# Kernel tuning notes

Hardware: AMD Instinct MI355X
Metric: run time of the kernel (lower is better)

The kernel has to match this reference:

```python
import jax, jax.numpy as jnp
import numpy as np

WS = 7   # window_size
SS = 3   # shift_size
NH = 6   # num_heads
EPS = 1e-5


def _partition(x, ws):
    # [b,h,w,c] -> [b*(h//ws)*(w//ws), ws*ws, c]
    b, h, w, c = x.shape
    x = x.reshape(b, h // ws, ws, w // ws, ws, c)
    return x.transpose(0, 1, 3, 2, 4, 5).reshape(-1, ws * ws, c)


def _reverse(windows, ws, h, w, b):
    c = windows.shape[-1]
    x = windows.reshape(b, h // ws, w // ws, ws, ws, c)
    return x.transpose(0, 1, 3, 2, 4, 5).reshape(b, h, w, c)


def _make_mask(h, w, ws, ss):
    # static (numpy) shifted-window attention mask, [nw, ws*ws, ws*ws]
    img = np.zeros((h, w), dtype=np.float32)
    slices = (slice(0, -ws), slice(-ws, -ss), slice(-ss, None))
    cnt = 0
    for hs in slices:
        for wsl in slices:
            img[hs, wsl] = cnt
            cnt += 1
    mw = img.reshape(h // ws, ws, w // ws, ws).transpose(0, 2, 1, 3).reshape(-1, ws * ws)
    am = mw[:, None, :] - mw[:, :, None]
    mask = np.where(am != 0, -100.0, 0.0).astype(np.float32)
    return jnp.asarray(mask)


def _layernorm(x, g, b):
    mu = jnp.mean(x, axis=-1, keepdims=True)
    var = jnp.var(x, axis=-1, keepdims=True)
    return (x - mu) * jax.lax.rsqrt(var + EPS) * g + b


def setup_inputs() -> dict:
    key = jax.random.key(0)
    ks = jax.random.split(key, 8)
    dim = 192
    s = lambda fan: 1.0 / np.sqrt(fan)
    return {
        "x": jax.random.normal(ks[0], (64, 56, 56, dim), dtype=jnp.float32),
        "n1_g": jnp.ones((dim,), jnp.float32),
        "n1_b": jnp.zeros((dim,), jnp.float32),
        "qkv_w": jax.random.normal(ks[1], (dim, 3 * dim), jnp.float32) * s(dim),
        "qkv_b": jnp.zeros((3 * dim,), jnp.float32),
        "proj_w": jax.random.normal(ks[2], (dim, dim), jnp.float32) * s(dim),
        "proj_b": jnp.zeros((dim,), jnp.float32),
        "n2_g": jnp.ones((dim,), jnp.float32),
        "n2_b": jnp.zeros((dim,), jnp.float32),
        "w1": jax.random.normal(ks[3], (dim, 4 * dim), jnp.float32) * s(dim),
        "b1": jnp.zeros((4 * dim,), jnp.float32),
        "w2": jax.random.normal(ks[4], (4 * dim, dim), jnp.float32) * s(4 * dim),
        "b2": jnp.zeros((dim,), jnp.float32),
    }


def reference(x, n1_g, n1_b, qkv_w, qkv_b, proj_w, proj_b, n2_g, n2_b, w1, b1, w2, b2):
    b, h, w, c = x.shape
    hd = c // NH
    scale = hd ** -0.5

    sc = x
    xn = _layernorm(x, n1_g, n1_b)
    sx = jnp.roll(xn, shift=(-SS, -SS), axis=(1, 2))

    xw = _partition(sx, WS)                      # [B_, n, c], n = WS*WS
    B_, n, _ = xw.shape

    qkv = xw @ qkv_w + qkv_b                      # [B_, n, 3c]
    qkv = qkv.reshape(B_, n, 3, NH, hd).transpose(2, 0, 3, 1, 4)
    q, k, v = qkv[0], qkv[1], qkv[2]              # [B_, NH, n, hd]

    attn = jnp.einsum("whnd,whmd->whnm", q, k) * scale   # [B_, NH, n, n]
    mask = _make_mask(h, w, WS, SS)               # [nw, n, n]
    nw = mask.shape[0]
    attn = attn.reshape(b // nw * 1 if False else b, nw, NH, n, n) if False else attn.reshape(B_ // nw, nw, NH, n, n)
    attn = attn + mask[None, :, None, :, :]
    attn = attn.reshape(-1, NH, n, n)
    attn = jax.nn.softmax(attn, axis=-1)

    out = jnp.einsum("whnm,whmd->whnd", attn, v)  # [B_, NH, n, hd]
    out = out.transpose(0, 2, 1, 3).reshape(B_, n, c)
    out = out @ proj_w + proj_b

    sx = _reverse(out, WS, h, w, b)
    xs = jnp.roll(sx, shift=(SS, SS), axis=(1, 2))

    x2 = sc + xs
    x2n = _layernorm(x2, n2_g, n2_b)
    mlp = jax.nn.gelu(x2n @ w1 + b1, approximate=False) @ w2 + b2
    return x2 + mlp
```

## Files before the change

kernel.cpp:

```cpp
#include <hip/hip_runtime.h>

typedef __attribute__((ext_vector_type(4))) float f32x4;
typedef __attribute__((ext_vector_type(8))) short bf16x8;
typedef __attribute__((ext_vector_type(2))) unsigned int u32x2;

#define NHEAD 6

__device__ __forceinline__ unsigned short f2bf(float f){
  union{float f;unsigned int u;}c; c.f=f;
  unsigned int x=c.u;
  return (unsigned short)((x + 0x7FFFu + ((x>>16)&1u)) >> 16);
}
__device__ __forceinline__ unsigned int cvtpk(float a, float b){
  unsigned int r;
  asm("v_cvt_pk_bf16_f32 %0, %1, %2" : "=v"(r) : "v"(a), "v"(b));
  return r;
}

__global__ void wt_kernel(const float* __restrict__ w, unsigned short* __restrict__ wt,
                          int K, int N){
  int idx = blockIdx.x*256 + threadIdx.x;
  if (idx >= K*N) return;
  int k = idx / N, n = idx - k*N;
  wt[(size_t)n*K + k] = f2bf(w[idx]);
}

template<int SHIFT>
__global__ __launch_bounds__(256) void ln_kernel(const float* __restrict__ x,
    const float* __restrict__ gw, const float* __restrict__ bw,
    unsigned short* __restrict__ out){
  int tok  = blockIdx.x*4 + (threadIdx.x>>6);
  int lane = threadIdx.x & 63;
  const float* row = x + (size_t)tok*192;
  float4 v = make_float4(0.f,0.f,0.f,0.f);
  if (lane < 48) v = *(const float4*)(row + lane*4);
  float s  = v.x+v.y+v.z+v.w;
  float s2 = v.x*v.x+v.y*v.y+v.z*v.z+v.w*v.w;
  #pragma unroll
  for (int off=32; off; off>>=1){ s += __shfl_xor(s,off); s2 += __shfl_xor(s2,off); }
  float mu = s*(1.f/192.f);
  float rs = rsqrtf(s2*(1.f/192.f) - mu*mu + 1e-5f);
  size_t otok;
  if (SHIFT){
    int b = tok/3136; int hw = tok - b*3136; int h = hw/56; int w = hw - h*56;
    int hs = h-3; if (hs<0) hs += 56;
    int wsh = w-3; if (wsh<0) wsh += 56;
    int wr = hs/7, r = hs - wr*7, wc = wsh/7, c = wsh - wc*7;
    otok = ((size_t)b*64 + wr*8 + wc)*49 + r*7 + c;
  } else {
    otok = (size_t)tok;
  }
  if (lane < 48){
    int cb = lane*4;
    float4 g4 = *(const float4*)(gw + cb);
    float4 b4 = *(const float4*)(bw + cb);
    u32x2 o;
    o.x = cvtpk((v.x-mu)*rs*g4.x + b4.x, (v.y-mu)*rs*g4.y + b4.y);
    o.y = cvtpk((v.z-mu)*rs*g4.z + b4.z, (v.w-mu)*rs*g4.w + b4.w);
    *(u32x2*)(out + otok*192 + cb) = o;
  }
}

enum { EPI_QKV=0, EPI_PROJ=1, EPI_GELU=2, EPI_FINAL=3 };

__device__ __forceinline__ float gelu_fast(float v){
  float t = v*(1.59576912f + 0.07135481f*v*v);
  float e = __expf(-t);
  return v/(1.f + e);
}

__device__ __forceinline__ size_t proj_rowbase(int grow){
  int winr = grow/49; int nn = grow - winr*49;
  int b  = winr>>6; int wi = winr&63; int wr_ = wi>>3; int wc_ = wi&7;
  int r7 = nn/7;  int c7 = nn - r7*7;
  int h = wr_*7 + r7 + 3; if (h>=56) h-=56;
  int w = wc_*7 + c7 + 3; if (w>=56) w-=56;
  return (((size_t)b*3136) + h*56 + w)*192;
}

template<int EPI>
__global__ __launch_bounds__(512) void gemm_k(
    const unsigned short* __restrict__ A,
    const unsigned short* __restrict__ BT,
    const float* __restrict__ bias,
    const float* __restrict__ res,
    void* __restrict__ Cout,
    int M, int N, int Nb, int K)
{
  __shared__ unsigned short lA[256*64];
  __shared__ unsigned short lB[64*64];
  const int tid  = threadIdx.x;
  const int wave = tid>>6, lane = tid&63;
  const int wm = wave>>1, wn = wave&1;
  const int lr = lane&15, lh = lane>>4;

  int bid = blockIdx.x;
  int yb = bid/(8*Nb); int rr = bid - yb*8*Nb; int xq = rr>>3; int y8 = rr&7;
  const int m0 = (yb*8 + y8)*256, n0 = xq*64;

  f32x4 zero = {0.f,0.f,0.f,0.f};
  f32x4 acc[4][2];
  #pragma unroll
  for (int i=0;i<4;i++){ acc[i][0]=zero; acc[i][1]=zero; }

  const int row8 = tid>>3;
  const int csw  = ((tid&7) ^ (row8&7))*8;
  const unsigned short* Ag = A  + (size_t)(m0 + row8)*K + csw;
  const unsigned short* Bg = BT + (size_t)(n0 + row8)*K + csw;

  for (int kt=0; kt<K; kt+=64){
    __syncthreads();
    #pragma unroll
    for (int i=0;i<4;i++){
      __builtin_amdgcn_global_load_lds(
        (const __attribute__((address_space(1))) void*)(Ag + (size_t)i*64*K + kt),
        (__attribute__((address_space(3))) void*)(lA + i*4096 + wave*512),
        16, 0, 0);
    }
    __builtin_amdgcn_global_load_lds(
      (const __attribute__((address_space(1))) void*)(Bg + kt),
      (__attribute__((address_space(3))) void*)(lB + wave*512),
      16, 0, 0);
    __syncthreads();

    bf16x8 af[4][2], bfv[2][2];
    #pragma unroll
    for (int mi=0;mi<4;mi++)
      #pragma unroll
      for (int ks=0;ks<2;ks++){
        int arow = wm*64+mi*16+lr;
        af[mi][ks] = *(const bf16x8*)&lA[arow*64 + (((ks*4+lh) ^ (lr&7))*8)];
      }
    #pragma unroll
    for (int ni=0;ni<2;ni++)
      #pragma unroll
      for (int ks=0;ks<2;ks++){
        int brow = wn*32+ni*16+lr;
        bfv[ni][ks] = *(const bf16x8*)&lB[brow*64 + (((ks*4+lh) ^ (lr&7))*8)];
      }
    #pragma unroll
    for (int mi=0;mi<4;mi++)
      #pragma unroll
      for (int ni=0;ni<2;ni++)
        #pragma unroll
        for (int ks=0;ks<2;ks++)
          acc[mi][ni] = __builtin_amdgcn_mfma_f32_16x16x32_bf16(
              bfv[ni][ks], af[mi][ks], acc[mi][ni], 0,0,0);
  }

  if (EPI == EPI_QKV || EPI == EPI_GELU){
    __syncthreads();
    #pragma unroll
    for (int mi=0;mi<4;mi++){
      int row = wm*64 + mi*16 + lr;
      #pragma unroll
      for (int ni=0;ni<2;ni++){
        int colb = n0 + wn*32 + ni*16 + lh*4;
        float4 bv4 = *(const float4*)(bias + colb);
        float v0 = acc[mi][ni][0] + bv4.x;
        float v1 = acc[mi][ni][1] + bv4.y;
        float v2 = acc[mi][ni][2] + bv4.z;
        float v3 = acc[mi][ni][3] + bv4.w;
        u32x2 st;
        if (EPI == EPI_GELU){
          st.x = cvtpk(gelu_fast(v0), gelu_fast(v1));
          st.y = cvtpk(gelu_fast(v2), gelu_fast(v3));
        } else {
          st.x = cvtpk(v0,v1); st.y = cvtpk(v2,v3);
        }
        int c16 = wn*4 + ni*2 + (lh>>1);
        int byte = row*128 + ((c16 ^ (row&7))*16) + (lh&1)*8;
        *(u32x2*)((char*)lA + byte) = st;
      }
    }
    __syncthreads();
    #pragma unroll
    for (int rnd=0; rnd<4; ++rnd){
      int row = rnd*64 + (tid>>3);
      int chunk = tid&7;
      uint4 vv = *(const uint4*)((const char*)lA + row*128 + ((chunk ^ (row&7))*16));
      int grow = m0 + row;
      if (EPI == EPI_GELU){
        *(uint4*)((unsigned short*)Cout + (size_t)grow*N + n0 + chunk*8) = vv;
      } else {
        int winr = grow/49; int nn = grow - winr*49;
        int gcol = n0 + chunk*8;
        int which = gcol/192; int rem = gcol - which*192;
        int head = rem>>5, d = rem&31;
        *(uint4*)((unsigned short*)Cout + (size_t)winr*28224 + (size_t)which*9408
                  + head*1568 + nn*32 + d) = vv;
      }
    }
  } else {
    float* Tf = (float*)lA;
    #pragma unroll
    for (int h=0; h<2; ++h){
      __syncthreads();
      if ((wave>>2) == h){
        #pragma unroll
        for (int mi=0;mi<4;mi++){
          int lrow = (wm&1)*64 + mi*16 + lr;
          #pragma unroll
          for (int ni=0;ni<2;ni++){
            int colb = n0 + wn*32 + ni*16 + lh*4;
            float4 bv4 = *(const float4*)(bias + colb);
            float4 val = make_float4(acc[mi][ni][0]+bv4.x, acc[mi][ni][1]+bv4.y,
                                     acc[mi][ni][2]+bv4.z, acc[mi][ni][3]+bv4.w);
            int c4 = wn*8 + ni*4 + lh;
            *(float4*)&Tf[lrow*64 + ((c4 ^ (lrow&15))*4)] = val;
          }
        }
      }
      __syncthreads();
      #pragma unroll
      for (int rnd=0; rnd<4; ++rnd){
        int lrow = rnd*32 + (tid>>4);
        int chunk = tid&15;
        float4 v = *(const float4*)&Tf[lrow*64 + ((chunk ^ (lrow&15))*4)];
        int grow = m0 + h*128 + lrow;
        size_t base;
        if (EPI == EPI_FINAL) base = (size_t)grow*N + n0 + chunk*4;
        else                  base = proj_rowbase(grow) + n0 + chunk*4;
        float4 rv = *(const float4*)(res + base);
        *(float4*)((float*)Cout + base) =
            make_float4(rv.x+v.x, rv.y+v.y, rv.z+v.z, rv.w+v.w);
      }
    }
  }
}

__global__ __launch_bounds__(256) void attn_kernel(const unsigned short* __restrict__ qkv,
                                                   unsigned short* __restrict__ aout){
  __shared__ __align__(16) unsigned short ldsQK[4][4096];
  __shared__ __align__(16) unsigned short ldsV[4][2048];
  const int wave = threadIdx.x>>6, lane = threadIdx.x&63;
  const int lr = lane&15, lh = lane>>4;
  const int unit = blockIdx.x*4 + wave;
  const int win  = unit/NHEAD, head = unit - win*NHEAD;

  unsigned short* Q  = ldsQK[wave];
  unsigned short* Kl = ldsQK[wave] + 2048;
  unsigned short* P  = ldsQK[wave];
  unsigned short* Vt = ldsV[wave];

  const size_t wbase = (size_t)win*28224 + (size_t)head*1568;
  const unsigned short* gQ = qkv + wbase;
  const unsigned short* gK = qkv + wbase + 9408;
  const unsigned short* gV = qkv + wbase + 18816;

  {
    uint4 z = make_uint4(0,0,0,0);
    #pragma unroll
    for (int i=0;i<4;i++) *(uint4*)&Vt[(i*64+lane)*8] = z;
  }

  #pragma unroll
  for (int i=0;i<4;i++){
    int idx = i*64 + lane;
    if (idx < 196){
      int row = idx>>2, blk = idx&3;
      int sb = (blk ^ (row&3) ^ ((row>>2)&3));
      uint4 dq = *(const uint4*)(gQ + idx*8);
      *(uint4*)&Q[row*32 + sb*8] = dq;
      uint4 dk = *(const uint4*)(gK + idx*8);
      *(uint4*)&Kl[row*32 + sb*8] = dk;
    }
  }
  #pragma unroll
  for (int i=0;i<4;i++){
    int idx = i*64 + lane;
    if (idx < 196){
      int row = idx>>2, d0 = (idx&3)*8;
      uint4 dv = *(const uint4*)(gV + idx*8);
      unsigned int wds[4] = {dv.x, dv.y, dv.z, dv.w};
      int rb = row>>3, re = row&7;
      #pragma unroll
      for (int j=0;j<8;j++){
        unsigned short t = (unsigned short)(wds[j>>1] >> ((j&1)*16));
        Vt[(d0+j)*64 + ((rb ^ j)*8) + re] = t;
      }
    }
  }

  bf16x8 kf[4], qf[4];
  #pragma unroll
  for (int t=0;t<4;t++){
    int row = t*16 + lr;
    int off = row*32 + ((lh ^ (row&3) ^ ((row>>2)&3))*8);
    kf[t] = *(const bf16x8*)&Kl[off];
    qf[t] = *(const bf16x8*)&Q[off];
  }

  f32x4 zero = {0.f,0.f,0.f,0.f};
  f32x4 S[4][4];
  #pragma unroll
  for (int mi=0;mi<4;mi++)
    #pragma unroll
    for (int ni=0;ni<4;ni++)
      S[mi][ni] = __builtin_amdgcn_mfma_f32_16x16x32_bf16(kf[mi], qf[ni], zero, 0,0,0);

  const int wi = win & 63, wr = wi>>3, wc = wi&7;
  const bool hasmask = (wr==7) || (wc==7);
  const float scale = 0.17677669529663687f;

  #pragma unroll
  for (int ni=0;ni<4;ni++){
    int q = ni*16 + lr;
    int idq = 0;
    if (hasmask){
      int qr = q/7, qc = q - qr*7;
      int ih = (wr==7) ? ((qr>=4)?2:1) : 0;
      int iw = (wc==7) ? ((qc>=4)?2:1) : 0;
      idq = ih*3 + iw;
    }
    #pragma unroll
    for (int mi=0;mi<4;mi++){
      #pragma unroll
      for (int r=0;r<4;r++){
        int key = mi*16 + lh*4 + r;
        float s;
        if (key >= 49) s = -1e30f;
        else {
          float add = 0.f;
          if (hasmask){
            int kr = key/7, kc = key - kr*7;
            int ih = (wr==7) ? ((kr>=4)?2:1) : 0;
            int iw = (wc==7) ? ((kc>=4)?2:1) : 0;
            add = ((ih*3+iw) == idq) ? 0.f : -100.f;
          }
          s = S[mi][ni][r]*scale + add;
        }
        S[mi][ni][r] = s;
      }
    }
    float m = -1e30f;
    #pragma unroll
    for (int mi=0;mi<4;mi++)
      #pragma unroll
      for (int r=0;r<4;r++) m = fmaxf(m, S[mi][ni][r]);
    m = fmaxf(m, __shfl_xor(m, 16));
    m = fmaxf(m, __shfl_xor(m, 32));
    float sum = 0.f;
    #pragma unroll
    for (int mi=0;mi<4;mi++)
      #pragma unroll
      for (int r=0;r<4;r++){
        float p = __expf(S[mi][ni][r] - m);
        S[mi][ni][r] = p; sum += p;
      }
    sum += __shfl_xor(sum, 16);
    sum += __shfl_xor(sum, 32);
    float inv = 1.f/sum;
    #pragma unroll
    for (int mi=0;mi<4;mi++){
      int keyb = mi*16 + lh*4;
      int blk = keyb>>3, e0 = keyb&7;
      int addr = q*64 + ((blk ^ (q&7))*8) + e0;
      *(unsigned int*)&P[addr]   = cvtpk(S[mi][ni][0]*inv, S[mi][ni][1]*inv);
      *(unsigned int*)&P[addr+2] = cvtpk(S[mi][ni][2]*inv, S[mi][ni][3]*inv);
    }
  }

  bf16x8 vf[2][2];
  #pragma unroll
  for (int mt=0;mt<2;mt++)
    #pragma unroll
    for (int ks=0;ks<2;ks++){
      int row = mt*16 + lr;
      vf[mt][ks] = *(const bf16x8*)&Vt[row*64 + (((ks*4+lh) ^ (row&7))*8)];
    }
  f32x4 O[2][4];
  #pragma unroll
  for (int ni=0;ni<4;ni++){
    int q = ni*16 + lr;
    bf16x8 pf0 = *(const bf16x8*)&P[q*64 + (((0*4+lh) ^ (q&7))*8)];
    bf16x8 pf1 = *(const bf16x8*)&P[q*64 + (((1*4+lh) ^ (q&7))*8)];
    #pragma unroll
    for (int mt=0;mt<2;mt++){
      f32x4 t = __builtin_amdgcn_mfma_f32_16x16x32_bf16(vf[mt][0], pf0, zero, 0,0,0);
      O[mt][ni] = __builtin_amdgcn_mfma_f32_16x16x32_bf16(vf[mt][1], pf1, t, 0,0,0);
    }
  }

  #pragma unroll
  for (int ni=0;ni<4;ni++){
    int q = ni*16 + lr;
    if (q < 49){
      size_t ob = ((size_t)win*49 + q)*192 + head*32 + lh*4;
      #pragma unroll
      for (int mt=0;mt<2;mt++){
        u32x2 st;
        st.x = cvtpk(O[mt][ni][0], O[mt][ni][1]);
        st.y = cvtpk(O[mt][ni][2], O[mt][ni][3]);
        *(u32x2*)(aout + ob + mt*16) = st;
      }
    }
  }
}

extern "C" void kernel_launch(void* const* d_in, const int* in_sizes, int n_in,
                              void* d_out, int out_size, void* d_ws, size_t ws_size,
                              hipStream_t stream){
  (void)in_sizes; (void)n_in; (void)out_size; (void)ws_size;
  const float* x      = (const float*)d_in[0];
  const float* n1_g   = (const float*)d_in[1];
  const float* n1_b   = (const float*)d_in[2];
  const float* qkv_w  = (const float*)d_in[3];
  const float* qkv_b  = (const float*)d_in[4];
  const float* proj_w = (const float*)d_in[5];
  const float* proj_b = (const float*)d_in[6];
  const float* n2_g   = (const float*)d_in[7];
  const float* n2_b   = (const float*)d_in[8];
  const float* w1     = (const float*)d_in[9];
  const float* b1     = (const float*)d_in[10];
  const float* w2     = (const float*)d_in[11];
  const float* b2     = (const float*)d_in[12];

  char* ws = (char*)d_ws;
  unsigned short* qkvT = (unsigned short*)(ws + 0);
  unsigned short* projT= (unsigned short*)(ws + 221184);
  unsigned short* w1T  = (unsigned short*)(ws + 294912);
  unsigned short* w2T  = (unsigned short*)(ws + 589824);
  unsigned short* bufA = (unsigned short*)(ws + 884736);
  unsigned short* bufB = (unsigned short*)(ws + 77955072);
  float*          x2   = (float*)        (ws + 386236416);
  float* out = (float*)d_out;
  const int M = 200704;

  wt_kernel<<<432,256,0,stream>>>(qkv_w, qkvT, 192, 576);
  wt_kernel<<<144,256,0,stream>>>(proj_w, projT, 192, 192);
  wt_kernel<<<576,256,0,stream>>>(w1,    w1T,  192, 768);
  wt_kernel<<<576,256,0,stream>>>(w2,    w2T,  768, 192);

  ln_kernel<1><<<50176,256,0,stream>>>(x, n1_g, n1_b, bufA);
  gemm_k<EPI_QKV  ><<< 9*784, 512,0,stream>>>(bufA, qkvT, qkv_b, nullptr, bufB, M, 576, 9, 192);
  attn_kernel<<<6144,256,0,stream>>>(bufB, bufA);
  gemm_k<EPI_PROJ ><<< 3*784, 512,0,stream>>>(bufA, projT, proj_b, x, x2, M, 192, 3, 192);
  ln_kernel<0><<<50176,256,0,stream>>>(x2, n2_g, n2_b, bufA);
  gemm_k<EPI_GELU ><<<12*784, 512,0,stream>>>(bufA, w1T, b1, nullptr, bufB, M, 768, 12, 192);
  gemm_k<EPI_FINAL><<< 3*784, 512,0,stream>>>(bufB, w2T, b2, x2, out, M, 192, 3, 768);
}
```

Measured before the change: 714.0 us.

## Fuse QKV projection GEMM into windowed attention kernel per window

Replaces the separate QKV GEMM and attention kernels with one kernel that processes one window per block. Six waves compute the 49x576 QKV projection with MFMA, read the weights straight from global memory, and write Q, K and transposed V into LDS, where each wave then runs attention for one head. This removes the round trip of the large QKV intermediate through global memory and one kernel launch. In exchange, weight tiles are re-read from global (L2) memory by every block, the M dimension is padded from 49 to 64 rows, and per-block LDS use is larger, which can lower occupancy.

```diff
diff --git a/kernel.cpp b/kernel.cpp
--- a/kernel.cpp
+++ b/kernel.cpp
@@ -61,7 +61,7 @@
   }
 }
 
-enum { EPI_QKV=0, EPI_PROJ=1, EPI_GELU=2, EPI_FINAL=3 };
+enum { EPI_PROJ=1, EPI_GELU=2, EPI_FINAL=3 };
 
 __device__ __forceinline__ float gelu_fast(float v){
   float t = v*(1.59576912f + 0.07135481f*v*v);
@@ -148,7 +148,7 @@
               bfv[ni][ks], af[mi][ks], acc[mi][ni], 0,0,0);
   }
 
-  if (EPI == EPI_QKV || EPI == EPI_GELU){
+  if (EPI == EPI_GELU){
     __syncthreads();
     #pragma unroll
     for (int mi=0;mi<4;mi++){
@@ -162,12 +162,8 @@
         float v2 = acc[mi][ni][2] + bv4.z;
         float v3 = acc[mi][ni][3] + bv4.w;
         u32x2 st;
-        if (EPI == EPI_GELU){
-          st.x = cvtpk(gelu_fast(v0), gelu_fast(v1));
-          st.y = cvtpk(gelu_fast(v2), gelu_fast(v3));
-        } else {
-          st.x = cvtpk(v0,v1); st.y = cvtpk(v2,v3);
-        }
+        st.x = cvtpk(gelu_fast(v0), gelu_fast(v1));
+        st.y = cvtpk(gelu_fast(v2), gelu_fast(v3));
         int c16 = wn*4 + ni*2 + (lh>>1);
         int byte = row*128 + ((c16 ^ (row&7))*16) + (lh&1)*8;
         *(u32x2*)((char*)lA + byte) = st;
@@ -180,16 +176,7 @@
       int chunk = tid&7;
       uint4 vv = *(const uint4*)((const char*)lA + row*128 + ((chunk ^ (row&7))*16));
       int grow = m0 + row;
-      if (EPI == EPI_GELU){
-        *(uint4*)((unsigned short*)Cout + (size_t)grow*N + n0 + chunk*8) = vv;
-      } else {
-        int winr = grow/49; int nn = grow - winr*49;
-        int gcol = n0 + chunk*8;
-        int which = gcol/192; int rem = gcol - which*192;
-        int head = rem>>5, d = rem&31;
-        *(uint4*)((unsigned short*)Cout + (size_t)winr*28224 + (size_t)which*9408
-                  + head*1568 + nn*32 + d) = vv;
-      }
+      *(uint4*)((unsigned short*)Cout + (size_t)grow*N + n0 + chunk*8) = vv;
     }
   } else {
     float* Tf = (float*)lA;
@@ -229,58 +216,96 @@
   }
 }
 
-__global__ __launch_bounds__(256) void attn_kernel(const unsigned short* __restrict__ qkv,
-                                                   unsigned short* __restrict__ aout){
-  __shared__ __align__(16) unsigned short ldsQK[4][4096];
-  __shared__ __align__(16) unsigned short ldsV[4][2048];
-  const int wave = threadIdx.x>>6, lane = threadIdx.x&63;
+__global__ __launch_bounds__(384) void qkv_attn(
+    const unsigned short* __restrict__ xw,
+    const unsigned short* __restrict__ qkvT,
+    const float* __restrict__ bias,
+    unsigned short* __restrict__ aout)
+{
+  __shared__ __align__(16) unsigned short smem[36864];
+  const int tid  = threadIdx.x;
+  const int wave = tid>>6, lane = tid&63;
   const int lr = lane&15, lh = lane>>4;
-  const int unit = blockIdx.x*4 + wave;
-  const int win  = unit/NHEAD, head = unit - win*NHEAD;
-
-  unsigned short* Q  = ldsQK[wave];
-  unsigned short* Kl = ldsQK[wave] + 2048;
-  unsigned short* P  = ldsQK[wave];
-  unsigned short* Vt = ldsV[wave];
-
-  const size_t wbase = (size_t)win*28224 + (size_t)head*1568;
-  const unsigned short* gQ = qkv + wbase;
-  const unsigned short* gK = qkv + wbase + 9408;
-  const unsigned short* gV = qkv + wbase + 18816;
-
-  {
-    uint4 z = make_uint4(0,0,0,0);
-    #pragma unroll
-    for (int i=0;i<4;i++) *(uint4*)&Vt[(i*64+lane)*8] = z;
-  }
-
-  #pragma unroll
-  for (int i=0;i<4;i++){
-    int idx = i*64 + lane;
-    if (idx < 196){
-      int row = idx>>2, blk = idx&3;
-      int sb = (blk ^ (row&3) ^ ((row>>2)&3));
-      uint4 dq = *(const uint4*)(gQ + idx*8);
-      *(uint4*)&Q[row*32 + sb*8] = dq;
-      uint4 dk = *(const uint4*)(gK + idx*8);
-      *(uint4*)&Kl[row*32 + sb*8] = dk;
-    }
-  }
-  #pragma unroll
-  for (int i=0;i<4;i++){
-    int idx = i*64 + lane;
-    if (idx < 196){
-      int row = idx>>2, d0 = (idx&3)*8;
-      uint4 dv = *(const uint4*)(gV + idx*8);
-      unsigned int wds[4] = {dv.x, dv.y, dv.z, dv.w};
-      int rb = row>>3, re = row&7;
-      #pragma unroll
-      for (int j=0;j<8;j++){
-        unsigned short t = (unsigned short)(wds[j>>1] >> ((j&1)*16));
-        Vt[(d0+j)*64 + ((rb ^ j)*8) + re] = t;
-      }
-    }
-  }
+  const int win = blockIdx.x;
+  unsigned short* xwl = smem;
+  const size_t xbase = (size_t)win*49*192;
+
+  #pragma unroll
+  for (int p=0; p<4; ++p){
+    int c = p*384 + tid;
+    int row = c/24, col = c - row*24;
+    unsigned short* dst = &xwl[row*192 + ((col ^ (row&7))*8)];
+    if (row < 49){
+      *(uint4*)dst = *(const uint4*)(xw + xbase + (size_t)row*192 + col*8);
+    } else {
+      *(uint4*)dst = make_uint4(0,0,0,0);
+    }
+  }
+  __syncthreads();
+
+  f32x4 zero = {0.f,0.f,0.f,0.f};
+  f32x4 acc[4][6];
+  #pragma unroll
+  for (int i=0;i<4;i++)
+    #pragma unroll
+    for (int j=0;j<6;j++) acc[i][j]=zero;
+  const int ncol0 = wave*96;
+
+  #pragma unroll
+  for (int kk=0; kk<6; ++kk){
+    bf16x8 af[4];
+    #pragma unroll
+    for (int mi=0;mi<4;mi++)
+      af[mi] = *(const bf16x8*)&xwl[(mi*16+lr)*192 + (((kk*4+lh) ^ (lr&7))*8)];
+    bf16x8 bfv[6];
+    #pragma unroll
+    for (int j=0;j<6;j++)
+      bfv[j] = *(const bf16x8*)(qkvT + (size_t)(ncol0 + j*16 + lr)*192 + kk*32 + lh*8);
+    #pragma unroll
+    for (int mi=0;mi<4;mi++)
+      #pragma unroll
+      for (int j=0;j<6;j++)
+        acc[mi][j] = __builtin_amdgcn_mfma_f32_16x16x32_bf16(
+            bfv[j], af[mi], acc[mi][j], 0,0,0);
+  }
+  __syncthreads();
+
+  const int which = wave>>1;
+  #pragma unroll
+  for (int j=0;j<6;j++){
+    int unit = j>>1, ni_u = j&1;
+    int head = (wave&1)*3 + unit;
+    int d0 = ni_u*16 + lh*4;
+    float4 bb = *(const float4*)(bias + which*192 + head*32 + d0);
+    #pragma unroll
+    for (int mi=0;mi<4;mi++){
+      int row = mi*16 + lr;
+      float v0 = acc[mi][j][0]+bb.x, v1 = acc[mi][j][1]+bb.y;
+      float v2 = acc[mi][j][2]+bb.z, v3 = acc[mi][j][3]+bb.w;
+      if (which < 2){
+        unsigned short* base = smem + head*4096 + which*2048;
+        int blk = d0>>3;
+        int sb = blk ^ (row&3) ^ ((row>>2)&3);
+        int addr = row*32 + sb*8 + (d0&7);
+        u32x2 st; st.x = cvtpk(v0,v1); st.y = cvtpk(v2,v3);
+        *(u32x2*)(base + addr) = st;
+      } else {
+        unsigned short* vt = smem + 24576 + head*2048;
+        int rb = row>>3, re = row&7;
+        vt[(d0+0)*64 + ((rb ^ ((d0+0)&7))*8) + re] = f2bf(v0);
+        vt[(d0+1)*64 + ((rb ^ ((d0+1)&7))*8) + re] = f2bf(v1);
+        vt[(d0+2)*64 + ((rb ^ ((d0+2)&7))*8) + re] = f2bf(v2);
+        vt[(d0+3)*64 + ((rb ^ ((d0+3)&7))*8) + re] = f2bf(v3);
+      }
+    }
+  }
+  __syncthreads();
+
+  const int head = wave;
+  unsigned short* Q  = smem + head*4096;
+  unsigned short* Kl = Q + 2048;
+  unsigned short* P  = Q;
+  unsigned short* Vt = smem + 24576 + head*2048;
 
   bf16x8 kf[4], qf[4];
   #pragma unroll
@@ -291,7 +316,6 @@
     qf[t] = *(const bf16x8*)&Q[off];
   }
 
-  f32x4 zero = {0.f,0.f,0.f,0.f};
   f32x4 S[4][4];
   #pragma unroll
   for (int mi=0;mi<4;mi++)
@@ -433,9 +457,8 @@
   wt_kernel<<<576,256,0,stream>>>(w2,    w2T,  768, 192);
 
   ln_kernel<1><<<50176,256,0,stream>>>(x, n1_g, n1_b, bufA);
-  gemm_k<EPI_QKV  ><<< 9*784, 512,0,stream>>>(bufA, qkvT, qkv_b, nullptr, bufB, M, 576, 9, 192);
-  attn_kernel<<<6144,256,0,stream>>>(bufB, bufA);
-  gemm_k<EPI_PROJ ><<< 3*784, 512,0,stream>>>(bufA, projT, proj_b, x, x2, M, 192, 3, 192);
+  qkv_attn<<<4096,384,0,stream>>>(bufA, qkvT, qkv_b, bufB);
+  gemm_k<EPI_PROJ ><<< 3*784, 512,0,stream>>>(bufB, projT, proj_b, x, x2, M, 192, 3, 192);
   ln_kernel<0><<<50176,256,0,stream>>>(x2, n2_g, n2_b, bufA);
   gemm_k<EPI_GELU ><<<12*784, 512,0,stream>>>(bufA, w1T, b1, nullptr, bufB, M, 768, 12, 192);
   gemm_k<EPI_FINAL><<< 3*784, 512,0,stream>>>(bufB, w2T, b2, x2, out, M, 192, 3, 768);
```

New measurement: 811.7 us. 1.14x slower.

## Chunk QKV/attention and MLP stages into quarters to keep intermediates cache-resident

Applied to the files above, without the earlier changes.

Splits the token batch into four chunks of 50176 rows. For each chunk it runs LN1, the QKV GEMM and attention, and later the fc1 and fc2 GEMMs, so the large qkv and hidden intermediates are about a quarter the size. The goal is for producer-consumer traffic to stay in the large last-level cache instead of going out to HBM. In exchange there are more kernel launches with smaller grids. The per-chunk GEMMs also drop the grouped block remap, which may hurt L2 reuse within each launch.

```diff
diff --git a/kernel.cpp b/kernel.cpp
--- a/kernel.cpp
+++ b/kernel.cpp
@@ -28,8 +28,8 @@
 template<int SHIFT>
 __global__ __launch_bounds__(256) void ln_kernel(const float* __restrict__ x,
     const float* __restrict__ gw, const float* __restrict__ bw,
-    unsigned short* __restrict__ out){
-  int tok  = blockIdx.x*4 + (threadIdx.x>>6);
+    unsigned short* __restrict__ out, int tok_off){
+  int tok  = tok_off + blockIdx.x*4 + (threadIdx.x>>6);
   int lane = threadIdx.x & 63;
   const float* row = x + (size_t)tok*192;
   float4 v = make_float4(0.f,0.f,0.f,0.f);
@@ -40,15 +40,15 @@
   for (int off=32; off; off>>=1){ s += __shfl_xor(s,off); s2 += __shfl_xor(s2,off); }
   float mu = s*(1.f/192.f);
   float rs = rsqrtf(s2*(1.f/192.f) - mu*mu + 1e-5f);
-  size_t otok;
+  long otok;
   if (SHIFT){
     int b = tok/3136; int hw = tok - b*3136; int h = hw/56; int w = hw - h*56;
     int hs = h-3; if (hs<0) hs += 56;
     int wsh = w-3; if (wsh<0) wsh += 56;
     int wr = hs/7, r = hs - wr*7, wc = wsh/7, c = wsh - wc*7;
-    otok = ((size_t)b*64 + wr*8 + wc)*49 + r*7 + c;
+    otok = ((long)b*64 + wr*8 + wc)*49 + r*7 + c;
   } else {
-    otok = (size_t)tok;
+    otok = (long)tok;
   }
   if (lane < 48){
     int cb = lane*4;
@@ -57,7 +57,7 @@
     u32x2 o;
     o.x = cvtpk((v.x-mu)*rs*g4.x + b4.x, (v.y-mu)*rs*g4.y + b4.y);
     o.y = cvtpk((v.z-mu)*rs*g4.z + b4.z, (v.w-mu)*rs*g4.w + b4.w);
-    *(u32x2*)(out + otok*192 + cb) = o;
+    *(u32x2*)(out + (size_t)(otok - tok_off)*192 + cb) = o;
   }
 }
 
@@ -78,14 +78,14 @@
   return (((size_t)b*3136) + h*56 + w)*192;
 }
 
-template<int EPI>
+template<int EPI, bool REMAP>
 __global__ __launch_bounds__(512) void gemm_k(
     const unsigned short* __restrict__ A,
     const unsigned short* __restrict__ BT,
     const float* __restrict__ bias,
     const float* __restrict__ res,
     void* __restrict__ Cout,
-    int M, int N, int Nb, int K)
+    int N, int Nb, int K)
 {
   __shared__ unsigned short lA[256*64];
   __shared__ unsigned short lB[64*64];
@@ -95,8 +95,14 @@
   const int lr = lane&15, lh = lane>>4;
 
   int bid = blockIdx.x;
-  int yb = bid/(8*Nb); int rr = bid - yb*8*Nb; int xq = rr>>3; int y8 = rr&7;
-  const int m0 = (yb*8 + y8)*256, n0 = xq*64;
+  int y, xq;
+  if (REMAP){
+    int yb = bid/(8*Nb); int rr = bid - yb*8*Nb; xq = rr>>3; int y8 = rr&7;
+    y = yb*8 + y8;
+  } else {
+    y = bid / Nb; xq = bid - y*Nb;
+  }
+  const int m0 = y*256, n0 = xq*64;
 
   f32x4 zero = {0.f,0.f,0.f,0.f};
   f32x4 acc[4][2];
@@ -230,7 +236,8 @@
 }
 
 __global__ __launch_bounds__(256) void attn_kernel(const unsigned short* __restrict__ qkv,
-                                                   unsigned short* __restrict__ aout){
+                                                   unsigned short* __restrict__ aout,
+                                                   int win_off){
   __shared__ __align__(16) unsigned short ldsQK[4][4096];
   __shared__ __align__(16) unsigned short ldsV[4][2048];
   const int wave = threadIdx.x>>6, lane = threadIdx.x&63;
@@ -386,7 +393,7 @@
   for (int ni=0;ni<4;ni++){
     int q = ni*16 + lr;
     if (q < 49){
-      size_t ob = ((size_t)win*49 + q)*192 + head*32 + lh*4;
+      size_t ob = ((size_t)(win_off + win)*49 + q)*192 + head*32 + lh*4;
       #pragma unroll
       for (int mt=0;mt<2;mt++){
         u32x2 st;
@@ -417,26 +424,37 @@
   const float* b2     = (const float*)d_in[12];
 
   char* ws = (char*)d_ws;
-  unsigned short* qkvT = (unsigned short*)(ws + 0);
-  unsigned short* projT= (unsigned short*)(ws + 221184);
-  unsigned short* w1T  = (unsigned short*)(ws + 294912);
-  unsigned short* w2T  = (unsigned short*)(ws + 589824);
-  unsigned short* bufA = (unsigned short*)(ws + 884736);
-  unsigned short* bufB = (unsigned short*)(ws + 77955072);
-  float*          x2   = (float*)        (ws + 386236416);
+  unsigned short* qkvT   = (unsigned short*)(ws + 0);
+  unsigned short* projT  = (unsigned short*)(ws + 221184);
+  unsigned short* w1T    = (unsigned short*)(ws + 294912);
+  unsigned short* w2T    = (unsigned short*)(ws + 589824);
+  unsigned short* xw_buf = (unsigned short*)(ws + 884736);
+  unsigned short* qkv_buf= (unsigned short*)(ws + 20152320);
+  unsigned short* attn_o = (unsigned short*)(ws + 77955072);
+  unsigned short* h_buf  = (unsigned short*)(ws + 155025408);
+  float*          x2     = (float*)        (ws + 232095744);
+  unsigned short* x2n    = (unsigned short*)(ws + 386236416);
   float* out = (float*)d_out;
-  const int M = 200704;
 
   wt_kernel<<<432,256,0,stream>>>(qkv_w, qkvT, 192, 576);
   wt_kernel<<<144,256,0,stream>>>(proj_w, projT, 192, 192);
   wt_kernel<<<576,256,0,stream>>>(w1,    w1T,  192, 768);
   wt_kernel<<<576,256,0,stream>>>(w2,    w2T,  768, 192);
 
-  ln_kernel<1><<<50176,256,0,stream>>>(x, n1_g, n1_b, bufA);
-  gemm_k<EPI_QKV  ><<< 9*784, 512,0,stream>>>(bufA, qkvT, qkv_b, nullptr, bufB, M, 576, 9, 192);
-  attn_kernel<<<6144,256,0,stream>>>(bufB, bufA);
-  gemm_k<EPI_PROJ ><<< 3*784, 512,0,stream>>>(bufA, projT, proj_b, x, x2, M, 192, 3, 192);
-  ln_kernel<0><<<50176,256,0,stream>>>(x2, n2_g, n2_b, bufA);
-  gemm_k<EPI_GELU ><<<12*784, 512,0,stream>>>(bufA, w1T, b1, nullptr, bufB, M, 768, 12, 192);
-  gemm_k<EPI_FINAL><<< 3*784, 512,0,stream>>>(bufB, w2T, b2, x2, out, M, 192, 3, 768);
-}
+  const int QROWS = 50176;
+  for (int q = 0; q < 4; ++q){
+    ln_kernel<1><<<QROWS/4, 256,0,stream>>>(x, n1_g, n1_b, xw_buf, q*QROWS);
+    gemm_k<EPI_QKV,false ><<<196*9, 512,0,stream>>>(xw_buf, qkvT, qkv_b, nullptr,
+                                                    qkv_buf, 576, 9, 192);
+    attn_kernel<<<1536,256,0,stream>>>(qkv_buf, attn_o, q*1024);
+  }
+  gemm_k<EPI_PROJ,true ><<<3*784, 512,0,stream>>>(attn_o, projT, proj_b, x, x2, 192, 3, 192);
+  ln_kernel<0><<<QROWS*4/4, 256,0,stream>>>(x2, n2_g, n2_b, x2n, 0);
+  for (int q = 0; q < 4; ++q){
+    size_t ro = (size_t)q*QROWS*192;
+    gemm_k<EPI_GELU,false ><<<196*12, 512,0,stream>>>(x2n + ro, w1T, b1, nullptr,
+                                                      h_buf, 768, 12, 192);
+    gemm_k<EPI_FINAL,false><<<196*3, 512,0,stream>>>(h_buf, w2T, b2, x2 + ro,
+                                                     out + ro, 192, 3, 768);
+  }
+}
```

Measured after the change: 881.6 us. 1.23x slower.
